# Optimization experiments

Hardware: AMD Instinct MI355X
Metric: run time of the kernel (lower is better)

The kernel has to match this reference:

```python
import jax, jax.numpy as jnp
import numpy as np

IN_CH, SKIP_CH, OUT_CH = 256, 128, 128
K2 = 9  # 3x3 deformable kernel
LK = 15  # large kernel for offset conv
EPS = 1e-5


def conv2d(x, w, b, pad):
    out = jax.lax.conv_general_dilated(
        x, w, (1, 1), ((pad[0], pad[0]), (pad[1], pad[1])),
        dimension_numbers=("NCHW", "OIHW", "NCHW"))
    return out + b[None, :, None, None]


def conv_transpose_2x2_s2(x, w, b):
    # torch ConvTranspose2d(k=2, s=2, pad=0); w: [in, out, 2, 2]
    wt = jnp.flip(w, (2, 3)).transpose(1, 0, 2, 3)  # [out, in, 2, 2]
    out = jax.lax.conv_general_dilated(
        x, wt, (1, 1), ((1, 1), (1, 1)), lhs_dilation=(2, 2),
        dimension_numbers=("NCHW", "OIHW", "NCHW"))
    return out + b[None, :, None, None]


def bn_relu(x, g, b):
    # training-mode BatchNorm2d (batch statistics) + ReLU
    m = jnp.mean(x, (0, 2, 3), keepdims=True)
    v = jnp.var(x, (0, 2, 3), keepdims=True)
    xn = (x - m) * jax.lax.rsqrt(v + EPS)
    return jax.nn.relu(xn * g[None, :, None, None] + b[None, :, None, None])


def deform_conv3x3(x, offset, mask, w):
    # torchvision DeformConv2d semantics, k=3, stride=1, pad=1, dil=1, no bias
    B, C, H, W = x.shape
    off = offset.reshape(B, K2, 2, H, W)
    dy, dx = off[:, :, 0], off[:, :, 1]            # [B, 9, H, W]
    ki = (jnp.arange(K2) // 3).astype(x.dtype)
    kj = (jnp.arange(K2) % 3).astype(x.dtype)
    hh = jnp.arange(H, dtype=x.dtype)
    ww = jnp.arange(W, dtype=x.dtype)
    y = dy + (hh[None, :, None] + ki[:, None, None] - 1.0)[None]   # [B,9,H,W]
    xx = dx + (ww[None, None, :] + kj[:, None, None] - 1.0)[None]
    y0 = jnp.floor(y)
    x0 = jnp.floor(xx)
    wy = y - y0   # bilinear weights
    wx = xx - x0
    y0i = y0.astype(jnp.int32)
    x0i = x0.astype(jnp.int32)
    x_flat = x.reshape(B, C, H * W)

    def gather(yc, xc):
        valid = ((yc >= 0) & (yc < H) & (xc >= 0) & (xc < W)).astype(x.dtype)
        idx = jnp.clip(yc, 0, H - 1) * W + jnp.clip(xc, 0, W - 1)
        g = jnp.take_along_axis(x_flat, idx.reshape(B, 1, -1), axis=2)
        return g.reshape(B, C, K2, H, W) * valid[:, None]

    v00 = gather(y0i, x0i)
    v01 = gather(y0i, x0i + 1)
    v10 = gather(y0i + 1, x0i)
    v11 = gather(y0i + 1, x0i + 1)
    wye = wy[:, None]
    wxe = wx[:, None]
    sampled = (v00 * (1 - wye) * (1 - wxe) + v01 * (1 - wye) * wxe
               + v10 * wye * (1 - wxe) + v11 * wye * wxe)
    sampled = sampled * mask[:, None]              # [B,C,9,H,W]
    return jnp.einsum("bckhw,ock->bohw", sampled, w.reshape(w.shape[0], C, K2))


def setup_inputs() -> dict:
    key = jax.random.key(0)
    ks = jax.random.split(key, 16)
    s = 0.02
    return {
        "x": jax.random.normal(ks[0], (2, IN_CH, 64, 64), jnp.float32),
        "skip": jax.random.normal(ks[1], (2, SKIP_CH, 128, 128), jnp.float32),
        "w_up": jax.random.normal(ks[2], (IN_CH, OUT_CH, 2, 2), jnp.float32) * s,
        "b_up": jnp.zeros((OUT_CH,), jnp.float32),
        "w_ref": jax.random.normal(ks[3], (OUT_CH, OUT_CH + SKIP_CH, 3, 3), jnp.float32) * s,
        "b_ref": jnp.zeros((OUT_CH,), jnp.float32),
        "g1": jnp.ones((OUT_CH,), jnp.float32),
        "be1": jnp.zeros((OUT_CH,), jnp.float32),
        "w_offh": jax.random.normal(ks[4], (2 * K2, OUT_CH, 1, LK), jnp.float32) * s,
        "b_offh": jnp.zeros((2 * K2,), jnp.float32),
        "w_offv": jax.random.normal(ks[5], (2 * K2, OUT_CH, LK, 1), jnp.float32) * s,
        "b_offv": jnp.zeros((2 * K2,), jnp.float32),
        "w_mask": jax.random.normal(ks[6], (K2, OUT_CH, 3, 3), jnp.float32) * s,
        "b_mask": jnp.zeros((K2,), jnp.float32),
        "w_def": jax.random.normal(ks[7], (OUT_CH, OUT_CH, 3, 3), jnp.float32) * s,
        "g2": jnp.ones((OUT_CH,), jnp.float32),
        "be2": jnp.zeros((OUT_CH,), jnp.float32),
    }


def reference(x, skip, w_up, b_up, w_ref, b_ref, g1, be1,
              w_offh, b_offh, w_offv, b_offv, w_mask, b_mask,
              w_def, g2, be2):
    xu = conv_transpose_2x2_s2(x, w_up, b_up)            # [B, out_ch, 2H, 2W]
    cat = jnp.concatenate([xu, skip], axis=1)
    h = bn_relu(conv2d(cat, w_ref, b_ref, (1, 1)), g1, be1)
    # DSConv: LDoffset = conv(1x15) + conv(15x1); sigmoid mask; deform conv; BN+ReLU
    offset = conv2d(h, w_offh, b_offh, (0, LK // 2)) + conv2d(h, w_offv, b_offv, (LK // 2, 0))
    mask = jax.nn.sigmoid(conv2d(h, w_mask, b_mask, (1, 1)))
    return bn_relu(deform_conv3x3(h, offset, mask, w_def), g2, be2)
```

## Files before the change

### kernel.cpp

```cpp
#include <hip/hip_runtime.h>
#include <hip/hip_bf16.h>

typedef __attribute__((ext_vector_type(8))) short bf16x8;
typedef __attribute__((ext_vector_type(4))) float f32x4;
typedef __attribute__((ext_vector_type(8))) unsigned short u16x8;

static __device__ __forceinline__ unsigned short f2bf(float f) {
  union { float f; unsigned u; } v; v.f = f;
  unsigned r = v.u + 0x7fff + ((v.u >> 16) & 1);
  return (unsigned short)(r >> 16);
}

__global__ void k_upsampleT(const float* __restrict__ x, const float* __restrict__ w_up,
                            const float* __restrict__ b_up, unsigned short* __restrict__ catT) {
  int bid = blockIdx.x;
  int wt = bid & 7;
  int hh = (bid >> 3) & 63;
  int b  = bid >> 9;
  int t = threadIdx.x;
  __shared__ float xs[256][8];
  int ww0 = wt * 8;
  int pix = t & 7, icb = t >> 3;
  #pragma unroll
  for (int r = 0; r < 8; ++r) {
    int ic = r * 32 + icb;
    xs[ic][pix] = x[((b * 256 + ic) * 64 + hh) * 64 + ww0 + pix];
  }
  __syncthreads();
  int oc = t & 127, g = t >> 7;
  float bias = b_up[oc];
  float acc0[8], acc1[8];
  #pragma unroll
  for (int p = 0; p < 8; ++p) { acc0[p] = bias; acc1[p] = bias; }
  for (int i = 0; i < 256; ++i) {
    float wv0 = w_up[((i * 128 + oc) * 2 + g) * 2 + 0];
    float wv1 = w_up[((i * 128 + oc) * 2 + g) * 2 + 1];
    #pragma unroll
    for (int p = 0; p < 8; ++p) {
      float xv = xs[i][p];
      acc0[p] += xv * wv0;
      acc1[p] += xv * wv1;
    }
  }
  int h = 2 * hh + g;
  int cg = oc >> 5, icl = oc & 31;
  long plane = ((long)(b * 8 + cg) << 14) + (h << 7);
  #pragma unroll
  for (int p = 0; p < 8; ++p) {
    int w0c = 2 * (ww0 + p);
    catT[((plane + w0c) << 5) + icl]     = f2bf(acc0[p]);
    catT[((plane + w0c + 1) << 5) + icl] = f2bf(acc1[p]);
  }
}

__global__ void k_skipT(const float* __restrict__ skip, unsigned short* __restrict__ catT) {
  int bid = blockIdx.x;
  int xb = bid & 1;
  int y  = (bid >> 1) & 127;
  int cg = (bid >> 8) & 3;
  int b  = bid >> 10;
  int t = threadIdx.x;
  __shared__ float ts[32][65];
  int x = t & 63, c4 = t >> 6, x0 = xb * 64;
  #pragma unroll
  for (int p = 0; p < 8; ++p) {
    int c = p * 4 + c4;
    ts[c][x] = skip[(((long)(b * 128 + cg * 32 + c)) << 14) + (y << 7) + x0 + x];
  }
  __syncthreads();
  int ic = t & 31, xg = t >> 5;
  long plane = ((long)(b * 8 + 4 + cg) << 14) + (y << 7) + x0;
  #pragma unroll
  for (int q = 0; q < 8; ++q) {
    int xx = xg * 8 + q;
    catT[((plane + xx) << 5) + ic] = f2bf(ts[ic][xx]);
  }
}

__global__ void k_wrefT(const float* __restrict__ wr, unsigned short* __restrict__ wbT) {
  int idx = blockIdx.x * 256 + threadIdx.x;
  int tap = idx >> 15;
  int rem = idx & 32767;
  int oc = rem >> 8, ic = rem & 255;
  wbT[idx] = f2bf(wr[(oc * 256 + ic) * 9 + tap]);
}

__global__ void k_womT(const float* __restrict__ wh, const float* __restrict__ wv,
                       const float* __restrict__ wm, unsigned short* __restrict__ wOM) {
  int idx = blockIdx.x * 256 + threadIdx.x;
  int tap = idx / 6144;
  int rem = idx - tap * 6144;
  int j = rem >> 7, ic = rem & 127;
  float v = 0.f;
  if (tap < 15) {
    if (j < 18) v = wh[(j * 128 + ic) * 15 + tap];
  } else if (tap < 30) {
    if (j < 18) v = wv[(j * 128 + ic) * 15 + (tap - 15)];
  } else {
    if (j >= 18 && j < 27) v = wm[((j - 18) * 128 + ic) * 9 + (tap - 30)];
  }
  wOM[idx] = f2bf(v);
}

__global__ void k_wdefA(const float* __restrict__ wd, unsigned short* __restrict__ wdefA) {
  int idx = blockIdx.x * 256 + threadIdx.x;
  if (idx >= 147456) return;
  int j   = idx & 7;
  int oc  = (idx >> 3) & 127;
  int lhi = (idx >> 10) & 3;
  int ks  = idx >> 12;
  int k = ks % 9, cg = ks / 9;
  int c = cg * 32 + lhi * 8 + j;
  wdefA[idx] = f2bf(wd[(oc * 128 + c) * 9 + k]);
}

__global__ __launch_bounds__(256, 2)
void k_conv3m(const unsigned short* __restrict__ catT, const unsigned short* __restrict__ wbT,
              const float* __restrict__ br, float* __restrict__ out) {
  int bid = blockIdx.x;
  int xt = bid & 1;
  int y  = (bid >> 1) & 127;
  int b  = bid >> 8;
  int x0 = xt * 64;
  int t = threadIdx.x;
  int l = t & 63, w = t >> 6;
  __shared__ unsigned short xs[3 * 66 * 40];
  f32x4 acc[2][4];
  #pragma unroll
  for (int m = 0; m < 2; ++m)
    #pragma unroll
    for (int n = 0; n < 4; ++n)
      #pragma unroll
      for (int r = 0; r < 4; ++r) acc[m][n][r] = 0.f;
  const unsigned short* catb = catT + ((long)b << 22);
  int lan15 = l & 15, lhi = l >> 4;
  for (int cg = 0; cg < 8; ++cg) {
    __syncthreads();
    for (int j = t; j < 792; j += 256) {
      int g = j & 3;
      int rc = j >> 2;
      int c = rc % 66, r = rc / 66;
      int gy = y + r - 1, gx = x0 + c - 1;
      u16x8 v = {0, 0, 0, 0, 0, 0, 0, 0};
      if ((unsigned)gy < 128u && (unsigned)gx < 128u)
        v = *(const u16x8*)(catb + ((((long)cg << 14) + (gy << 7) + gx) << 5) + g * 8);
      *(u16x8*)(xs + (r * 66 + c) * 40 + g * 8) = v;
    }
    bf16x8 af[2][9];
    int kbase = cg * 32 + lhi * 8;
    #pragma unroll
    for (int mt = 0; mt < 2; ++mt)
      #pragma unroll
      for (int tap = 0; tap < 9; ++tap)
        af[mt][tap] = *(const bf16x8*)(wbT + ((tap * 128 + w * 32 + mt * 16 + lan15) * 256 + kbase));
    __syncthreads();
    #pragma unroll
    for (int tap = 0; tap < 9; ++tap) {
      int ky = tap / 3, kx = tap % 3;
      #pragma unroll
      for (int nt = 0; nt < 4; ++nt) {
        int c = nt * 16 + lan15 + kx;
        bf16x8 bfv = *(const bf16x8*)(xs + ((ky * 66 + c) * 40) + lhi * 8);
        acc[0][nt] = __builtin_amdgcn_mfma_f32_16x16x32_bf16(af[0][tap], bfv, acc[0][nt], 0, 0, 0);
        acc[1][nt] = __builtin_amdgcn_mfma_f32_16x16x32_bf16(af[1][tap], bfv, acc[1][nt], 0, 0, 0);
      }
    }
  }
  #pragma unroll
  for (int mt = 0; mt < 2; ++mt)
    #pragma unroll
    for (int reg = 0; reg < 4; ++reg) {
      int oc = w * 32 + mt * 16 + lhi * 4 + reg;
      float bias = br[oc];
      long obase = ((long)(b * 128 + oc) << 14) + (y << 7);
      #pragma unroll
      for (int nt = 0; nt < 4; ++nt)
        out[obase + x0 + nt * 16 + lan15] = acc[mt][nt][reg] + bias;
    }
}

__global__ void k_bnstats(const float* __restrict__ src, float* __restrict__ mean,
                          float* __restrict__ rstd) {
  int c = blockIdx.x, t = threadIdx.x;
  float s = 0.f, s2 = 0.f;
  for (int b = 0; b < 2; ++b) {
    const float4* p4 = (const float4*)(src + ((long)(b * 128 + c) << 14));
    for (int i = t; i < 4096; i += 256) {
      float4 v = p4[i];
      s  += v.x + v.y + v.z + v.w;
      s2 += v.x * v.x + v.y * v.y + v.z * v.z + v.w * v.w;
    }
  }
  #pragma unroll
  for (int off = 32; off; off >>= 1) {
    s  += __shfl_down(s, off);
    s2 += __shfl_down(s2, off);
  }
  __shared__ float as[4], as2[4];
  int wid = t >> 6;
  if ((t & 63) == 0) { as[wid] = s; as2[wid] = s2; }
  __syncthreads();
  if (t == 0) {
    float S = as[0] + as[1] + as[2] + as[3];
    float S2 = as2[0] + as2[1] + as2[2] + as2[3];
    float m = S / 32768.f;
    float var = S2 / 32768.f - m * m;
    mean[c] = m;
    rstd[c] = rsqrtf(var + 1e-5f);
  }
}

__global__ void k_bnrelu2(const float* __restrict__ tmp1, const float* __restrict__ mean,
                          const float* __restrict__ rstd, const float* __restrict__ g,
                          const float* __restrict__ be, unsigned short* __restrict__ hbufT) {
  int bid = blockIdx.x;
  int xb = bid & 1;
  int y  = (bid >> 1) & 127;
  int cg = (bid >> 8) & 3;
  int b  = bid >> 10;
  int t = threadIdx.x;
  __shared__ float ts[32][65];
  int x = t & 63, c4 = t >> 6, x0 = xb * 64;
  #pragma unroll
  for (int p = 0; p < 8; ++p) {
    int c = p * 4 + c4;
    int ch = cg * 32 + c;
    float sc = rstd[ch] * g[ch];
    float bb = be[ch] - mean[ch] * sc;
    long idx = ((long)(b * 128 + ch) << 14) + (y << 7) + x0 + x;
    ts[c][x] = fmaxf(tmp1[idx] * sc + bb, 0.f);
  }
  __syncthreads();
  int ic = t & 31, xg = t >> 5;
  long plane = ((long)(b * 4 + cg) << 14) + (y << 7) + x0;
  #pragma unroll
  for (int q = 0; q < 8; ++q) {
    int xx = xg * 8 + q;
    hbufT[((plane + xx) << 5) + ic] = f2bf(ts[ic][xx]);
  }
}

__global__ __launch_bounds__(256, 2)
void k_offmasks(const unsigned short* __restrict__ hbufT, const unsigned short* __restrict__ wOM,
                const float* __restrict__ bh, const float* __restrict__ bv,
                const float* __restrict__ bm,
                float* __restrict__ off, float* __restrict__ msk) {
  int bid = blockIdx.x;
  int swz = (bid & 7) * 64 + (bid >> 3);
  int b   = swz >> 8;
  int px0 = (swz & 255) * 64;
  int t = threadIdx.x;
  int l = t & 63, w = t >> 6;
  int lan15 = l & 15, lhi = l >> 4;
  int px = px0 + w * 16;
  int y = px >> 7, x0 = px & 127;
  int x = x0 + lan15;

  __shared__ unsigned short As[4 * 32 * 128];

  f32x4 acc0, acc1;
  #pragma unroll
  for (int r = 0; r < 4; ++r) { acc0[r] = 0.f; acc1[r] = 0.f; }

  const unsigned short* hb = hbufT + ((long)b << 21);
  const u16x8 z = {0, 0, 0, 0, 0, 0, 0, 0};
  int swz0 = (lan15 & 7) << 3;

  for (int grp = 0; grp < 10; ++grp) {
    int tap0 = grp * 4;
    __syncthreads();
    #pragma unroll
    for (int it = 0; it < 8; ++it) {
      int i = it * 256 + t;
      int tl = i >> 9, rem = i & 511;
      int j = rem >> 4, g16 = rem & 15;
      int tap = tap0 + tl;
      u16x8 v = z;
      if (tap < 39) v = *(const u16x8*)(wOM + ((tap * 48 + j) << 7) + g16 * 8);
      *(u16x8*)(As + tl * 4096 + j * 128 + ((g16 ^ (j & 7)) << 3)) = v;
    }
    __syncthreads();
    #pragma unroll
    for (int tl = 0; tl < 4; ++tl) {
      int tap = tap0 + tl;
      if (tap < 39) {
        int ky = (tap < 15) ? 0 : ((tap < 30) ? (tap - 22) : ((tap - 30) / 3 - 1));
        int kx = (tap < 15) ? (tap - 7) : ((tap < 30) ? 0 : ((tap - 30) % 3 - 1));
        int gy = y + ky, gx = x + kx;
        bool valid = ((unsigned)gy < 128u) & ((unsigned)gx < 128u);
        const unsigned short* bp = hb + ((((long)(gy << 7) + gx) << 5) + lhi * 8);
        bool do0 = tap < 30;
        const unsigned short* a0base = As + tl * 4096 + lan15 * 128;
        const unsigned short* a1base = a0base + 16 * 128;
        #pragma unroll
        for (int cg = 0; cg < 4; ++cg) {
          u16x8 bv8 = valid ? *(const u16x8*)(bp + ((long)cg << 19)) : z;
          bf16x8 bf = (bf16x8)bv8;
          int aoff = (((cg << 2) + lhi) ^ (lan15 & 7)) << 3;
          acc1 = __builtin_amdgcn_mfma_f32_16x16x32_bf16(*(const bf16x8*)(a1base + aoff),
                                                         bf, acc1, 0, 0, 0);
          if (do0)
            acc0 = __builtin_amdgcn_mfma_f32_16x16x32_bf16(*(const bf16x8*)(a0base + aoff),
                                                           bf, acc0, 0, 0, 0);
        }
      }
    }
  }

  int sp = (y << 7) + x;
  #pragma unroll
  for (int reg = 0; reg < 4; ++reg) {
    int j0 = lhi * 4 + reg;
    off[((long)(b * 18 + j0) << 14) + sp] = acc0[reg] + bh[j0] + bv[j0];
    int j1 = 16 + lhi * 4 + reg;
    float v = acc1[reg];
    if (j1 < 18) {
      off[((long)(b * 18 + j1) << 14) + sp] = v + bh[j1] + bv[j1];
    } else if (j1 < 27) {
      int jm = j1 - 18;
      msk[((long)(b * 9 + jm) << 14) + sp] = 1.f / (1.f + expf(-(v + bm[jm])));
    }
  }
}

__global__ __launch_bounds__(256, 2)
void k_deformm(const unsigned short* __restrict__ hbufT, const float* __restrict__ off,
               const float* __restrict__ msk, const unsigned short* __restrict__ wdefA,
               float* __restrict__ out) {
  int bid = blockIdx.x;
  int xt = bid & 3;
  int h  = (bid >> 2) & 127;
  int b  = bid >> 9;
  int w0 = xt * 32;
  int t = threadIdx.x;
  int l = t & 63, w = t >> 6;
  int lan15 = l & 15, lhi = l >> 4;

  __shared__ __align__(16) unsigned short S[9][32][40];
  __shared__ int   p_y0[288], p_x0[288];
  __shared__ float p_w00[288], p_w01[288], p_w10[288], p_w11[288];

  for (int idx = t; idx < 288; idx += 256) {
    int k = idx >> 5, pix = idx & 31;
    int sp = (h << 7) + w0 + pix;
    float dy = off[((long)(b * 18 + 2 * k) << 14) + sp];
    float dx = off[((long)(b * 18 + 2 * k + 1) << 14) + sp];
    float m  = msk[((long)(b * 9 + k) << 14) + sp];
    float y  = dy + (float)(h + k / 3 - 1);
    float xx = dx + (float)(w0 + pix + (k % 3) - 1);
    float y0f = floorf(y), x0f = floorf(xx);
    float wy = y - y0f, wx = xx - x0f;
    p_y0[idx] = (int)y0f; p_x0[idx] = (int)x0f;
    p_w00[idx] = (1.f - wy) * (1.f - wx) * m;
    p_w01[idx] = (1.f - wy) * wx * m;
    p_w10[idx] = wy * (1.f - wx) * m;
    p_w11[idx] = wy * wx * m;
  }

  f32x4 acc[2][2];
  #pragma unroll
  for (int m = 0; m < 2; ++m)
    #pragma unroll
    for (int n = 0; n < 2; ++n)
      #pragma unroll
      for (int r = 0; r < 4; ++r) acc[m][n][r] = 0.f;

  for (int cg = 0; cg < 4; ++cg) {
    __syncthreads();
    const unsigned short* hb = hbufT + (((long)(b * 4 + cg)) << 19);
    for (int idx = t; idx < 1152; idx += 256) {
      int cq = idx & 3, pix = (idx >> 2) & 31, k = idx >> 7;
      int kp = (k << 5) + pix;
      int y0 = p_y0[kp], x0 = p_x0[kp];
      float c00 = p_w00[kp], c01 = p_w01[kp], c10 = p_w10[kp], c11 = p_w11[kp];
      bool yi0 = (unsigned)y0 < 128u, yi1 = (unsigned)(y0 + 1) < 128u;
      bool xi0 = (unsigned)x0 < 128u, xi1 = (unsigned)(x0 + 1) < 128u;
      const unsigned short* pbase = hb + ((((long)(y0 << 7) + x0) << 5) + cq * 8);
      u16x8 z = {0, 0, 0, 0, 0, 0, 0, 0};
      u16x8 v00 = (yi0 && xi0) ? *(const u16x8*)pbase          : z;
      u16x8 v01 = (yi0 && xi1) ? *(const u16x8*)(pbase + 32)   : z;
      u16x8 v10 = (yi1 && xi0) ? *(const u16x8*)(pbase + 4096) : z;
      u16x8 v11 = (yi1 && xi1) ? *(const u16x8*)(pbase + 4128) : z;
      u16x8 o;
      #pragma unroll
      for (int j = 0; j < 8; ++j) {
        float s = c00 * __uint_as_float((unsigned)(unsigned short)v00[j] << 16)
                + c01 * __uint_as_float((unsigned)(unsigned short)v01[j] << 16)
                + c10 * __uint_as_float((unsigned)(unsigned short)v10[j] << 16)
                + c11 * __uint_as_float((unsigned)(unsigned short)v11[j] << 16);
        o[j] = f2bf(s);
      }
      *(u16x8*)(&S[k][pix][cq * 8]) = o;
    }
    bf16x8 af0[9], af1[9];
    #pragma unroll
    for (int k = 0; k < 9; ++k) {
      long wbase = ((((long)(cg * 9 + k) * 4 + lhi) * 128) + w * 32 + lan15) * 8;
      af0[k] = *(const bf16x8*)(wdefA + wbase);
      af1[k] = *(const bf16x8*)(wdefA + wbase + 128);
    }
    __syncthreads();
    #pragma unroll
    for (int k = 0; k < 9; ++k) {
      #pragma unroll
      for (int nt = 0; nt < 2; ++nt) {
        bf16x8 bfv = *(const bf16x8*)(&S[k][nt * 16 + lan15][lhi * 8]);
        acc[0][nt] = __builtin_amdgcn_mfma_f32_16x16x32_bf16(af0[k], bfv, acc[0][nt], 0, 0, 0);
        acc[1][nt] = __builtin_amdgcn_mfma_f32_16x16x32_bf16(af1[k], bfv, acc[1][nt], 0, 0, 0);
      }
    }
  }
  #pragma unroll
  for (int mt = 0; mt < 2; ++mt)
    #pragma unroll
    for (int reg = 0; reg < 4; ++reg) {
      int oc = w * 32 + mt * 16 + lhi * 4 + reg;
      long obase = ((long)(b * 128 + oc) << 14) + (h << 7) + w0;
      out[obase + lan15]      = acc[mt][0][reg];
      out[obase + 16 + lan15] = acc[mt][1][reg];
    }
}

__global__ void k_bnrelu(const float4* __restrict__ src, const float* __restrict__ mean,
                         const float* __restrict__ rstd, const float* __restrict__ g,
                         const float* __restrict__ be, float4* __restrict__ dst) {
  int i = blockIdx.x * 256 + threadIdx.x;
  if (i >= 1048576) return;
  int c = (i >> 12) & 127;
  float sc = rstd[c] * g[c];
  float bb = be[c] - mean[c] * sc;
  float4 v = src[i];
  v.x = fmaxf(v.x * sc + bb, 0.f);
  v.y = fmaxf(v.y * sc + bb, 0.f);
  v.z = fmaxf(v.z * sc + bb, 0.f);
  v.w = fmaxf(v.w * sc + bb, 0.f);
  dst[i] = v;
}

extern "C" void kernel_launch(void* const* d_in, const int* in_sizes, int n_in,
                              void* d_out, int out_size, void* d_ws, size_t ws_size,
                              hipStream_t stream) {
  const float* x      = (const float*)d_in[0];
  const float* skip   = (const float*)d_in[1];
  const float* w_up   = (const float*)d_in[2];
  const float* b_up   = (const float*)d_in[3];
  const float* w_ref  = (const float*)d_in[4];
  const float* b_ref  = (const float*)d_in[5];
  const float* g1     = (const float*)d_in[6];
  const float* be1    = (const float*)d_in[7];
  const float* w_offh = (const float*)d_in[8];
  const float* b_offh = (const float*)d_in[9];
  const float* w_offv = (const float*)d_in[10];
  const float* b_offv = (const float*)d_in[11];
  const float* w_mask = (const float*)d_in[12];
  const float* b_mask = (const float*)d_in[13];
  const float* w_def  = (const float*)d_in[14];
  const float* g2     = (const float*)d_in[15];
  const float* be2    = (const float*)d_in[16];

  char* W = (char*)d_ws;
  unsigned short* catT  = (unsigned short*)W;
  float*          tmp1  = (float*)(W + 16777216);
  unsigned short* hbufT = (unsigned short*)(W + 33554432);
  float*          offb  = (float*)(W + 41943040);
  float*          mskb  = (float*)(W + 44302336);
  float*          stat  = (float*)(W + 45481984);
  unsigned short* wbT   = (unsigned short*)(W + 45484032);
  unsigned short* wOM   = (unsigned short*)(W + 46073856);
  unsigned short* wdefA = (unsigned short*)(W + 46553088);
  float*          dpre  = (float*)W;

  hipLaunchKernelGGL(k_wrefT, dim3(1152), dim3(256), 0, stream, w_ref, wbT);
  hipLaunchKernelGGL(k_womT, dim3(936), dim3(256), 0, stream, w_offh, w_offv, w_mask, wOM);
  hipLaunchKernelGGL(k_wdefA, dim3(576), dim3(256), 0, stream, w_def, wdefA);
  hipLaunchKernelGGL(k_upsampleT, dim3(1024), dim3(256), 0, stream, x, w_up, b_up, catT);
  hipLaunchKernelGGL(k_skipT, dim3(2048), dim3(256), 0, stream, skip, catT);
  hipLaunchKernelGGL(k_conv3m, dim3(512), dim3(256), 0, stream, catT, wbT, b_ref, tmp1);
  hipLaunchKernelGGL(k_bnstats, dim3(128), dim3(256), 0, stream, tmp1, stat, stat + 128);
  hipLaunchKernelGGL(k_bnrelu2, dim3(2048), dim3(256), 0, stream, tmp1, stat, stat + 128,
                     g1, be1, hbufT);
  hipLaunchKernelGGL(k_offmasks, dim3(512), dim3(256), 0, stream, hbufT, wOM,
                     b_offh, b_offv, b_mask, offb, mskb);
  hipLaunchKernelGGL(k_deformm, dim3(1024), dim3(256), 0, stream, hbufT, offb, mskb,
                     wdefA, dpre);
  hipLaunchKernelGGL(k_bnstats, dim3(128), dim3(256), 0, stream, dpre, stat + 256, stat + 384);
  hipLaunchKernelGGL(k_bnrelu, dim3(4096), dim3(256), 0, stream,
                     (const float4*)dpre, stat + 256, stat + 384, g2, be2, (float4*)d_out);
}
```

Baseline: 201.1 us.

## Use MFMA for transposed-conv upsample and widen conv3 tiles with prefetch

Replaces the scalar FP32 transposed-conv upsample with a bf16 MFMA kernel, adding a small kernel that pre-packs the upsample weights to bf16. Rewrites the 3x3 refine conv so each block covers a full 128-pixel row, with register-staged prefetch of the next channel group overlapping the MFMA work. The aim is to cut the upsample's FP32 ALU cost and to amortize weight loads and global latency in conv3. In exchange, the upsample drops to bf16 input precision, conv3 runs with half as many blocks at occupancy 1, and register pressure rises.

```diff
diff --git a/kernel.cpp b/kernel.cpp
--- a/kernel.cpp
+++ b/kernel.cpp
@@ -11,45 +11,78 @@
   return (unsigned short)(r >> 16);
 }
 
-__global__ void k_upsampleT(const float* __restrict__ x, const float* __restrict__ w_up,
-                            const float* __restrict__ b_up, unsigned short* __restrict__ catT) {
+__global__ void k_wupA(const float* __restrict__ wu, unsigned short* __restrict__ wupA) {
+  int idx = blockIdx.x * 256 + threadIdx.x;
+  int ic = idx & 255, oc = (idx >> 8) & 127, tap = idx >> 15;
+  wupA[idx] = f2bf(wu[(ic * 128 + oc) * 4 + tap]);
+}
+
+__global__ __launch_bounds__(256, 2)
+void k_upsampleM(const float* __restrict__ x, const unsigned short* __restrict__ wupA,
+                 const float* __restrict__ b_up, unsigned short* __restrict__ catT) {
   int bid = blockIdx.x;
-  int wt = bid & 7;
-  int hh = (bid >> 3) & 63;
-  int b  = bid >> 9;
+  int half = bid & 1;
+  int hh = (bid >> 1) & 63;
+  int b  = bid >> 7;
+  int ww0 = half * 32;
   int t = threadIdx.x;
-  __shared__ float xs[256][8];
-  int ww0 = wt * 8;
-  int pix = t & 7, icb = t >> 3;
-  #pragma unroll
-  for (int r = 0; r < 8; ++r) {
-    int ic = r * 32 + icb;
-    xs[ic][pix] = x[((b * 256 + ic) * 64 + hh) * 64 + ww0 + pix];
+  int l = t & 63, w = t >> 6;
+  int kh = w >> 1, kw = w & 1;
+  int lan15 = l & 15, lhi = l >> 4;
+  __shared__ unsigned short xs[32][264];
+
+  {
+    int ic = t;
+    const float4* xp = (const float4*)(x + (((long)(b * 256 + ic)) << 12) + (hh << 6) + ww0);
+    #pragma unroll
+    for (int q = 0; q < 8; ++q) {
+      float4 v = xp[q];
+      xs[q * 4 + 0][ic] = f2bf(v.x);
+      xs[q * 4 + 1][ic] = f2bf(v.y);
+      xs[q * 4 + 2][ic] = f2bf(v.z);
+      xs[q * 4 + 3][ic] = f2bf(v.w);
+    }
   }
   __syncthreads();
-  int oc = t & 127, g = t >> 7;
-  float bias = b_up[oc];
-  float acc0[8], acc1[8];
-  #pragma unroll
-  for (int p = 0; p < 8; ++p) { acc0[p] = bias; acc1[p] = bias; }
-  for (int i = 0; i < 256; ++i) {
-    float wv0 = w_up[((i * 128 + oc) * 2 + g) * 2 + 0];
-    float wv1 = w_up[((i * 128 + oc) * 2 + g) * 2 + 1];
-    #pragma unroll
-    for (int p = 0; p < 8; ++p) {
-      float xv = xs[i][p];
-      acc0[p] += xv * wv0;
-      acc1[p] += xv * wv1;
-    }
-  }
-  int h = 2 * hh + g;
-  int cg = oc >> 5, icl = oc & 31;
-  long plane = ((long)(b * 8 + cg) << 14) + (h << 7);
-  #pragma unroll
-  for (int p = 0; p < 8; ++p) {
-    int w0c = 2 * (ww0 + p);
-    catT[((plane + w0c) << 5) + icl]     = f2bf(acc0[p]);
-    catT[((plane + w0c + 1) << 5) + icl] = f2bf(acc1[p]);
+
+  f32x4 acc[8][2];
+  #pragma unroll
+  for (int m = 0; m < 8; ++m)
+    #pragma unroll
+    for (int n = 0; n < 2; ++n)
+      #pragma unroll
+      for (int r = 0; r < 4; ++r) acc[m][n][r] = 0.f;
+
+  const unsigned short* ab = wupA + ((w * 128 + lan15) << 8) + lhi * 8;
+  #pragma unroll
+  for (int kc = 0; kc < 8; ++kc) {
+    bf16x8 b0 = *(const bf16x8*)(&xs[lan15][kc * 32 + lhi * 8]);
+    bf16x8 b1 = *(const bf16x8*)(&xs[16 + lan15][kc * 32 + lhi * 8]);
+    #pragma unroll
+    for (int mt = 0; mt < 8; ++mt) {
+      bf16x8 af = *(const bf16x8*)(ab + (mt << 12) + kc * 32);
+      acc[mt][0] = __builtin_amdgcn_mfma_f32_16x16x32_bf16(af, b0, acc[mt][0], 0, 0, 0);
+      acc[mt][1] = __builtin_amdgcn_mfma_f32_16x16x32_bf16(af, b1, acc[mt][1], 0, 0, 0);
+    }
+  }
+
+  int oh = 2 * hh + kh;
+  #pragma unroll
+  for (int mt = 0; mt < 8; ++mt) {
+    int ocb = mt * 16 + lhi * 4;
+    float4 bias = *(const float4*)(b_up + ocb);
+    int cg = ocb >> 5, icl = ocb & 31;
+    long plane = ((long)(b * 8 + cg) << 14) + (oh << 7);
+    #pragma unroll
+    for (int nt = 0; nt < 2; ++nt) {
+      int ow = 2 * (ww0 + nt * 16 + lan15) + kw;
+      unsigned u0 = (unsigned)f2bf(acc[mt][nt][0] + bias.x)
+                  | ((unsigned)f2bf(acc[mt][nt][1] + bias.y) << 16);
+      unsigned u1 = (unsigned)f2bf(acc[mt][nt][2] + bias.z)
+                  | ((unsigned)f2bf(acc[mt][nt][3] + bias.w) << 16);
+      uint2 pk; pk.x = u0; pk.y = u1;
+      *(uint2*)(catT + ((plane + ow) << 5) + icl) = pk;
+    }
   }
 }
 
@@ -114,58 +147,88 @@
   wdefA[idx] = f2bf(wd[(oc * 128 + c) * 9 + k]);
 }
 
-__global__ __launch_bounds__(256, 2)
-void k_conv3m(const unsigned short* __restrict__ catT, const unsigned short* __restrict__ wbT,
+__global__ __launch_bounds__(256, 1)
+void k_conv3r(const unsigned short* __restrict__ catT, const unsigned short* __restrict__ wbT,
               const float* __restrict__ br, float* __restrict__ out) {
   int bid = blockIdx.x;
-  int xt = bid & 1;
-  int y  = (bid >> 1) & 127;
-  int b  = bid >> 8;
-  int x0 = xt * 64;
+  int y = bid & 127, b = bid >> 7;
   int t = threadIdx.x;
   int l = t & 63, w = t >> 6;
-  __shared__ unsigned short xs[3 * 66 * 40];
-  f32x4 acc[2][4];
+  int lan15 = l & 15, lhi = l >> 4;
+  __shared__ unsigned short xs[3 * 130 * 40];
+  const u16x8 z = {0, 0, 0, 0, 0, 0, 0, 0};
+  f32x4 acc[2][8];
   #pragma unroll
   for (int m = 0; m < 2; ++m)
     #pragma unroll
-    for (int n = 0; n < 4; ++n)
+    for (int n = 0; n < 8; ++n)
       #pragma unroll
       for (int r = 0; r < 4; ++r) acc[m][n][r] = 0.f;
   const unsigned short* catb = catT + ((long)b << 22);
-  int lan15 = l & 15, lhi = l >> 4;
+
+  #pragma unroll
+  for (int it = 0; it < 7; ++it) {
+    int idx = it * 256 + t;
+    if (idx < 1560) {
+      int g = idx & 3, rc = idx >> 2;
+      int r = rc / 130, c = rc - r * 130;
+      int gy = y + r - 1, gx = c - 1;
+      u16x8 v = z;
+      if ((unsigned)gy < 128u && (unsigned)gx < 128u)
+        v = *(const u16x8*)(catb + (((long)(gy << 7) + gx) << 5) + g * 8);
+      *(u16x8*)(xs + (r * 130 + c) * 40 + g * 8) = v;
+    }
+  }
+  __syncthreads();
+
   for (int cg = 0; cg < 8; ++cg) {
-    __syncthreads();
-    for (int j = t; j < 792; j += 256) {
-      int g = j & 3;
-      int rc = j >> 2;
-      int c = rc % 66, r = rc / 66;
-      int gy = y + r - 1, gx = x0 + c - 1;
-      u16x8 v = {0, 0, 0, 0, 0, 0, 0, 0};
-      if ((unsigned)gy < 128u && (unsigned)gx < 128u)
-        v = *(const u16x8*)(catb + ((((long)cg << 14) + (gy << 7) + gx) << 5) + g * 8);
-      *(u16x8*)(xs + (r * 66 + c) * 40 + g * 8) = v;
+    u16x8 pre[7];
+    if (cg < 7) {
+      #pragma unroll
+      for (int it = 0; it < 7; ++it) {
+        int idx = it * 256 + t;
+        pre[it] = z;
+        if (idx < 1560) {
+          int g = idx & 3, rc = idx >> 2;
+          int r = rc / 130, c = rc - r * 130;
+          int gy = y + r - 1, gx = c - 1;
+          if ((unsigned)gy < 128u && (unsigned)gx < 128u)
+            pre[it] = *(const u16x8*)(catb + ((((long)(cg + 1) << 14) + (gy << 7) + gx) << 5) + g * 8);
+        }
+      }
     }
     bf16x8 af[2][9];
-    int kbase = cg * 32 + lhi * 8;
     #pragma unroll
     for (int mt = 0; mt < 2; ++mt)
       #pragma unroll
       for (int tap = 0; tap < 9; ++tap)
-        af[mt][tap] = *(const bf16x8*)(wbT + ((tap * 128 + w * 32 + mt * 16 + lan15) * 256 + kbase));
-    __syncthreads();
+        af[mt][tap] = *(const bf16x8*)(wbT + ((tap * 128 + w * 32 + mt * 16 + lan15) << 8) + cg * 32 + lhi * 8);
     #pragma unroll
     for (int tap = 0; tap < 9; ++tap) {
       int ky = tap / 3, kx = tap % 3;
       #pragma unroll
-      for (int nt = 0; nt < 4; ++nt) {
+      for (int nt = 0; nt < 8; ++nt) {
         int c = nt * 16 + lan15 + kx;
-        bf16x8 bfv = *(const bf16x8*)(xs + ((ky * 66 + c) * 40) + lhi * 8);
+        bf16x8 bfv = *(const bf16x8*)(xs + (ky * 130 + c) * 40 + lhi * 8);
         acc[0][nt] = __builtin_amdgcn_mfma_f32_16x16x32_bf16(af[0][tap], bfv, acc[0][nt], 0, 0, 0);
         acc[1][nt] = __builtin_amdgcn_mfma_f32_16x16x32_bf16(af[1][tap], bfv, acc[1][nt], 0, 0, 0);
       }
     }
-  }
+    __syncthreads();
+    if (cg < 7) {
+      #pragma unroll
+      for (int it = 0; it < 7; ++it) {
+        int idx = it * 256 + t;
+        if (idx < 1560) {
+          int g = idx & 3, rc = idx >> 2;
+          int r = rc / 130, c = rc - r * 130;
+          *(u16x8*)(xs + (r * 130 + c) * 40 + g * 8) = pre[it];
+        }
+      }
+      __syncthreads();
+    }
+  }
+
   #pragma unroll
   for (int mt = 0; mt < 2; ++mt)
     #pragma unroll
@@ -174,8 +237,8 @@
       float bias = br[oc];
       long obase = ((long)(b * 128 + oc) << 14) + (y << 7);
       #pragma unroll
-      for (int nt = 0; nt < 4; ++nt)
-        out[obase + x0 + nt * 16 + lan15] = acc[mt][nt][reg] + bias;
+      for (int nt = 0; nt < 8; ++nt)
+        out[obase + nt * 16 + lan15] = acc[mt][nt][reg] + bias;
     }
 }
 
@@ -264,7 +327,6 @@
 
   const unsigned short* hb = hbufT + ((long)b << 21);
   const u16x8 z = {0, 0, 0, 0, 0, 0, 0, 0};
-  int swz0 = (lan15 & 7) << 3;
 
   for (int grp = 0; grp < 10; ++grp) {
     int tap0 = grp * 4;
@@ -468,14 +530,16 @@
   unsigned short* wbT   = (unsigned short*)(W + 45484032);
   unsigned short* wOM   = (unsigned short*)(W + 46073856);
   unsigned short* wdefA = (unsigned short*)(W + 46553088);
+  unsigned short* wupA  = (unsigned short*)(W + 46848000);
   float*          dpre  = (float*)W;
 
   hipLaunchKernelGGL(k_wrefT, dim3(1152), dim3(256), 0, stream, w_ref, wbT);
   hipLaunchKernelGGL(k_womT, dim3(936), dim3(256), 0, stream, w_offh, w_offv, w_mask, wOM);
   hipLaunchKernelGGL(k_wdefA, dim3(576), dim3(256), 0, stream, w_def, wdefA);
-  hipLaunchKernelGGL(k_upsampleT, dim3(1024), dim3(256), 0, stream, x, w_up, b_up, catT);
+  hipLaunchKernelGGL(k_wupA, dim3(512), dim3(256), 0, stream, w_up, wupA);
+  hipLaunchKernelGGL(k_upsampleM, dim3(256), dim3(256), 0, stream, x, wupA, b_up, catT);
   hipLaunchKernelGGL(k_skipT, dim3(2048), dim3(256), 0, stream, skip, catT);
-  hipLaunchKernelGGL(k_conv3m, dim3(512), dim3(256), 0, stream, catT, wbT, b_ref, tmp1);
+  hipLaunchKernelGGL(k_conv3r, dim3(256), dim3(256), 0, stream, catT, wbT, b_ref, tmp1);
   hipLaunchKernelGGL(k_bnstats, dim3(128), dim3(256), 0, stream, tmp1, stat, stat + 128);
   hipLaunchKernelGGL(k_bnrelu2, dim3(2048), dim3(256), 0, stream, tmp1, stat, stat + 128,
                      g1, be1, hbufT);
```

After: 187.1 us. -7.0%, faster.
